# Kernel tuning notes

Hardware: AMD Instinct MI355X
Metric: run time of the kernel (lower is better)

## Reference

```python
import jax, jax.numpy as jnp
import numpy as np

N_NODES = 100000
N_FEAT = 128
N_EDGES = 640000
BATCH_SIZE = 50000


def setup_inputs() -> dict:
    key = jax.random.key(0)
    k1, k2 = jax.random.split(key)
    x = jax.random.normal(k1, (N_NODES, N_FEAT), dtype=jnp.float32)
    edge_index = jax.random.randint(k2, (2, N_EDGES), 0, N_NODES, dtype=jnp.int32)
    return {"x": x, "edge_index": edge_index, "batch_size": BATCH_SIZE}


def reference(x, edge_index, batch_size):
    # Filter edges whose destination is inside the target batch, then
    # scatter-sum source node features into destination rows (SpMM with a
    # 0/1 adjacency), matching adj.t().matmul(x) in the original.
    src = edge_index[0]
    dst = edge_index[1]
    valid = dst < batch_size                                  # [E]
    # Route invalid edges to a dummy segment (batch_size) and zero their values.
    seg = jnp.where(valid, dst, batch_size)                   # [E]
    vals = x[src] * valid[:, None].astype(x.dtype)            # [E, F] gather
    x_neighbors_sum = jax.ops.segment_sum(
        vals, seg, num_segments=batch_size + 1)[:batch_size]  # [B, F]
    node_labels = jnp.concatenate(
        [x[:batch_size, :], x_neighbors_sum], axis=-1)        # [B, 2F]
    return node_labels
```

## Files before the change

kernel.cpp:

```cpp
#include <hip/hip_runtime.h>

#define NFEAT 128
#define CAP 32
#define OVF_CAP 4096


__global__ void zero_kernel(int* __restrict__ p, int n) {
    int t = blockIdx.x * blockDim.x + threadIdx.x;
    if (t < n) p[t] = 0;
}

__global__ void bin_kernel(const int* __restrict__ src, const int* __restrict__ dst,
                           int* __restrict__ cnt, int* __restrict__ ovf_cnt,
                           int* __restrict__ ovf, int* __restrict__ bucket,
                           int E, int B) {
    int e = blockIdx.x * blockDim.x + threadIdx.x;
    if (e >= E) return;
    int d = dst[e];
    if (d >= B) return;
    int s = src[e];
    int pos = atomicAdd(&cnt[d], 1);
    if (pos < CAP) {
        bucket[d * CAP + pos] = s;
    } else {
        int o = atomicAdd(ovf_cnt, 1);
        if (o < OVF_CAP) { ovf[2 * o] = s; ovf[2 * o + 1] = d; }
    }
}

__global__ void aggregate_kernel(const float2* __restrict__ x2,
                                 const int* __restrict__ cnt,
                                 const int* __restrict__ bucket,
                                 float2* __restrict__ out2, int B) {
    int w = (blockIdx.x * blockDim.x + threadIdx.x) >> 6;
    int lane = threadIdx.x & 63;
    if (w >= B) return;
    int k = cnt[w];
    if (k > CAP) k = CAP;
    int sid = (lane < k) ? bucket[w * CAP + lane] : 0;
    float2 xd = x2[(size_t)w * 64 + lane];
    float2 acc = make_float2(0.f, 0.f);
    int j = 0;
    for (; j + 4 <= k; j += 4) {
        int s0 = __shfl(sid, j,     64);
        int s1 = __shfl(sid, j + 1, 64);
        int s2 = __shfl(sid, j + 2, 64);
        int s3 = __shfl(sid, j + 3, 64);
        float2 v0 = x2[(size_t)s0 * 64 + lane];
        float2 v1 = x2[(size_t)s1 * 64 + lane];
        float2 v2 = x2[(size_t)s2 * 64 + lane];
        float2 v3 = x2[(size_t)s3 * 64 + lane];
        acc.x += (v0.x + v1.x) + (v2.x + v3.x);
        acc.y += (v0.y + v1.y) + (v2.y + v3.y);
    }
    for (; j < k; ++j) {
        int s = __shfl(sid, j, 64);
        float2 v = x2[(size_t)s * 64 + lane];
        acc.x += v.x; acc.y += v.y;
    }
    size_t o = (size_t)w * 128;
    out2[o + lane] = xd;
    out2[o + 64 + lane] = acc;
}

__global__ void ovf_apply_kernel(const float* __restrict__ x,
                                 const int* __restrict__ ovf_cnt,
                                 const int* __restrict__ ovf,
                                 float* __restrict__ out, int B) {
    int n = *ovf_cnt;
    if (n > OVF_CAP) n = OVF_CAP;
    int t = blockIdx.x * blockDim.x + threadIdx.x;
    int e = t >> 5;
    if (e >= n) return;
    int c = t & 31;
    int s = ovf[2 * e], d = ovf[2 * e + 1];
    const float4 v = ((const float4*)(x + (size_t)s * NFEAT))[c];
    float* o = out + (size_t)d * 256 + NFEAT + c * 4;
    unsafeAtomicAdd(o + 0, v.x);
    unsafeAtomicAdd(o + 1, v.y);
    unsafeAtomicAdd(o + 2, v.z);
    unsafeAtomicAdd(o + 3, v.w);
}

__global__ void hist_kernel(const int* __restrict__ dst, int* __restrict__ cnt,
                            int E, int B) {
    int e = blockIdx.x * blockDim.x + threadIdx.x;
    if (e >= E) return;
    int d = dst[e];
    if (d < B) atomicAdd(&cnt[d], 1);
}

__global__ void alloc_kernel(const int* __restrict__ cnt, int* __restrict__ off,
                             int* __restrict__ deg, int* __restrict__ cursor, int B) {
    int t = blockIdx.x * blockDim.x + threadIdx.x;
    int lane = threadIdx.x & 63;
    int c = (t < B) ? cnt[t] : 0;
    int v = c;
    #pragma unroll
    for (int d = 1; d < 64; d <<= 1) {
        int n = __shfl_up(v, d, 64);
        if (lane >= d) v += n;
    }
    int total = __shfl(v, 63, 64);
    int base = 0;
    if (lane == 63 && total > 0) base = atomicAdd(cursor, total);
    base = __shfl(base, 63, 64);
    if (t < B) { off[t] = base + v - c; deg[t] = c; }
}

__global__ void scatter_kernel(const int* __restrict__ src, const int* __restrict__ dst,
                               int* __restrict__ cnt, const int* __restrict__ off,
                               int* __restrict__ bucket, int E, int B) {
    int e = blockIdx.x * blockDim.x + threadIdx.x;
    if (e >= E) return;
    int d = dst[e];
    if (d >= B) return;
    int old = atomicSub(&cnt[d], 1);
    bucket[off[d] + old - 1] = src[e];
}

__global__ void aggregate_csr_kernel(const float2* __restrict__ x2,
                                     const int* __restrict__ off, const int* __restrict__ deg,
                                     const int* __restrict__ bucket,
                                     float2* __restrict__ out2, int B) {
    int w = (blockIdx.x * blockDim.x + threadIdx.x) >> 6;
    int lane = threadIdx.x & 63;
    if (w >= B) return;
    int base = off[w];
    int k = deg[w];
    float2 acc = make_float2(0.f, 0.f);
    for (int j = 0; j < k; ++j) {
        int s = bucket[base + j];
        float2 v = x2[(size_t)s * 64 + lane];
        acc.x += v.x; acc.y += v.y;
    }
    float2 xd = x2[(size_t)w * 64 + lane];
    size_t o = (size_t)w * 128;
    out2[o + lane] = xd;
    out2[o + 64 + lane] = acc;
}

extern "C" void kernel_launch(void* const* d_in, const int* in_sizes, int n_in,
                              void* d_out, int out_size, void* d_ws, size_t ws_size,
                              hipStream_t stream) {
    const float* x  = (const float*)d_in[0];
    const int*   ei = (const int*)d_in[1];
    const int E = in_sizes[1] / 2;
    const int B = out_size / (2 * NFEAT);
    float* out = (float*)d_out;
    const int* src = ei;
    const int* dst = ei + E;

    size_t need_bin = ((size_t)B * (CAP + 1) + 1 + 2 * OVF_CAP) * sizeof(int);
    size_t need_csr = ((size_t)3 * B + 1 + E) * sizeof(int);

    if (ws_size >= need_bin) {
        int* cnt     = (int*)d_ws;
        int* ovf_cnt = cnt + B;
        int* ovf     = ovf_cnt + 1;
        int* bucket  = ovf + 2 * OVF_CAP;

        int nz = B + 1;
        zero_kernel<<<(nz + 255) / 256, 256, 0, stream>>>(cnt, nz);
        bin_kernel<<<(E + 255) / 256, 256, 0, stream>>>(src, dst, cnt, ovf_cnt, ovf, bucket, E, B);
        aggregate_kernel<<<(B + 3) / 4, 256, 0, stream>>>(
            (const float2*)x, cnt, bucket, (float2*)out, B);
        ovf_apply_kernel<<<(OVF_CAP * 32 + 255) / 256, 256, 0, stream>>>(x, ovf_cnt, ovf, out, B);
    } else {
        int* cnt    = (int*)d_ws;
        int* off    = cnt + B;
        int* deg    = off + B;
        int* cursor = deg + B;
        int* bucket = cursor + 1;
        int nz = 3 * B + 1;
        zero_kernel<<<(nz + 255) / 256, 256, 0, stream>>>(cnt, nz);
        hist_kernel<<<(E + 255) / 256, 256, 0, stream>>>(dst, cnt, E, B);
        alloc_kernel<<<(B + 255) / 256, 256, 0, stream>>>(cnt, off, deg, cursor, B);
        scatter_kernel<<<(E + 255) / 256, 256, 0, stream>>>(src, dst, cnt, off, bucket, E, B);
        aggregate_csr_kernel<<<(B + 3) / 4, 256, 0, stream>>>(
            (const float2*)x, off, deg, bucket, (float2*)out, B);
    }
}
```

Baseline: 140.7 us.

## Vectorize binning loads and process two rows per wavefront with float4 gathers

The bin kernel now handles four edges per thread using int4 loads of src and dst. The aggregate kernel splits each 64-lane wavefront into two halves, each gathering one destination row with float4 loads, so every load instruction moves more bytes and each wave covers two rows. Outputs are written with nontemporal stores. The cost is divergence when the two rows in a wave have different degrees, since both halves loop to the larger count, and the bin kernel runs with fewer threads, each issuing several atomics.

```diff
diff --git a/kernel.cpp b/kernel.cpp
--- a/kernel.cpp
+++ b/kernel.cpp
@@ -3,6 +3,8 @@
 #define NFEAT 128
 #define CAP 32
 #define OVF_CAP 4096
+
+typedef float vfloat4 __attribute__((ext_vector_type(4)));
 
 
 __global__ void zero_kernel(int* __restrict__ p, int n) {
@@ -14,53 +16,92 @@
                            int* __restrict__ cnt, int* __restrict__ ovf_cnt,
                            int* __restrict__ ovf, int* __restrict__ bucket,
                            int E, int B) {
-    int e = blockIdx.x * blockDim.x + threadIdx.x;
-    if (e >= E) return;
-    int d = dst[e];
-    if (d >= B) return;
-    int s = src[e];
-    int pos = atomicAdd(&cnt[d], 1);
-    if (pos < CAP) {
-        bucket[d * CAP + pos] = s;
+    int t = blockIdx.x * blockDim.x + threadIdx.x;
+    int e0 = t << 2;
+    if (e0 >= E) return;
+    if (e0 + 4 <= E) {
+        const int4 d4 = *(const int4*)(dst + e0);
+        const int4 s4 = *(const int4*)(src + e0);
+        int dd[4] = {d4.x, d4.y, d4.z, d4.w};
+        int ss[4] = {s4.x, s4.y, s4.z, s4.w};
+        #pragma unroll
+        for (int i = 0; i < 4; ++i) {
+            int d = dd[i];
+            if (d >= B) continue;
+            int pos = atomicAdd(&cnt[d], 1);
+            if (pos < CAP) {
+                bucket[d * CAP + pos] = ss[i];
+            } else {
+                int o = atomicAdd(ovf_cnt, 1);
+                if (o < OVF_CAP) { ovf[2 * o] = ss[i]; ovf[2 * o + 1] = d; }
+            }
+        }
     } else {
-        int o = atomicAdd(ovf_cnt, 1);
-        if (o < OVF_CAP) { ovf[2 * o] = s; ovf[2 * o + 1] = d; }
-    }
-}
-
-__global__ void aggregate_kernel(const float2* __restrict__ x2,
+        for (int e = e0; e < E; ++e) {
+            int d = dst[e];
+            if (d >= B) continue;
+            int pos = atomicAdd(&cnt[d], 1);
+            if (pos < CAP) {
+                bucket[d * CAP + pos] = src[e];
+            } else {
+                int o = atomicAdd(ovf_cnt, 1);
+                if (o < OVF_CAP) { ovf[2 * o] = src[e]; ovf[2 * o + 1] = d; }
+            }
+        }
+    }
+}
+
+__global__ void aggregate_kernel(const float4* __restrict__ x4,
                                  const int* __restrict__ cnt,
                                  const int* __restrict__ bucket,
-                                 float2* __restrict__ out2, int B) {
-    int w = (blockIdx.x * blockDim.x + threadIdx.x) >> 6;
+                                 float4* __restrict__ out4, int B) {
+    int wv   = (blockIdx.x * blockDim.x + threadIdx.x) >> 6;
     int lane = threadIdx.x & 63;
-    if (w >= B) return;
-    int k = cnt[w];
-    if (k > CAP) k = CAP;
-    int sid = (lane < k) ? bucket[w * CAP + lane] : 0;
-    float2 xd = x2[(size_t)w * 64 + lane];
-    float2 acc = make_float2(0.f, 0.f);
+    int h    = lane >> 5;
+    int l    = lane & 31;
+    int w0   = wv * 2;
+    if (w0 >= B) return;
+    int row   = w0 + h;
+    bool rowok = row < B;
+
+    int k = 0;
+    if (rowok) { k = cnt[row]; if (k > CAP) k = CAP; }
+    int sid = (l < k) ? bucket[(size_t)w0 * CAP + lane] : 0;
+    float4 xd = rowok ? x4[(size_t)row * 32 + l] : make_float4(0.f, 0.f, 0.f, 0.f);
+
+    int ko   = __shfl(k, lane ^ 32, 64);
+    int kmax = k > ko ? k : ko;
+
+    float4 acc = make_float4(0.f, 0.f, 0.f, 0.f);
+    int hb = h << 5;
     int j = 0;
-    for (; j + 4 <= k; j += 4) {
-        int s0 = __shfl(sid, j,     64);
-        int s1 = __shfl(sid, j + 1, 64);
-        int s2 = __shfl(sid, j + 2, 64);
-        int s3 = __shfl(sid, j + 3, 64);
-        float2 v0 = x2[(size_t)s0 * 64 + lane];
-        float2 v1 = x2[(size_t)s1 * 64 + lane];
-        float2 v2 = x2[(size_t)s2 * 64 + lane];
-        float2 v3 = x2[(size_t)s3 * 64 + lane];
-        acc.x += (v0.x + v1.x) + (v2.x + v3.x);
-        acc.y += (v0.y + v1.y) + (v2.y + v3.y);
-    }
-    for (; j < k; ++j) {
-        int s = __shfl(sid, j, 64);
-        float2 v = x2[(size_t)s * 64 + lane];
-        acc.x += v.x; acc.y += v.y;
-    }
-    size_t o = (size_t)w * 128;
-    out2[o + lane] = xd;
-    out2[o + 64 + lane] = acc;
+    for (; j + 4 <= kmax; j += 4) {
+        int s0 = __shfl(sid, hb + j,     64);
+        int s1 = __shfl(sid, hb + j + 1, 64);
+        int s2 = __shfl(sid, hb + j + 2, 64);
+        int s3 = __shfl(sid, hb + j + 3, 64);
+        float4 v0 = x4[(size_t)s0 * 32 + l];
+        float4 v1 = x4[(size_t)s1 * 32 + l];
+        float4 v2 = x4[(size_t)s2 * 32 + l];
+        float4 v3 = x4[(size_t)s3 * 32 + l];
+        if (j + 1 <= k) { acc.x += v0.x; acc.y += v0.y; acc.z += v0.z; acc.w += v0.w; }
+        if (j + 2 <= k) { acc.x += v1.x; acc.y += v1.y; acc.z += v1.z; acc.w += v1.w; }
+        if (j + 3 <= k) { acc.x += v2.x; acc.y += v2.y; acc.z += v2.z; acc.w += v2.w; }
+        if (j + 4 <= k) { acc.x += v3.x; acc.y += v3.y; acc.z += v3.z; acc.w += v3.w; }
+    }
+    for (; j < kmax; ++j) {
+        int s = __shfl(sid, hb + j, 64);
+        float4 v = x4[(size_t)s * 32 + l];
+        if (j < k) { acc.x += v.x; acc.y += v.y; acc.z += v.z; acc.w += v.w; }
+    }
+
+    if (rowok) {
+        size_t o = (size_t)row * 64;
+        vfloat4 xdn  = {xd.x, xd.y, xd.z, xd.w};
+        vfloat4 accn = {acc.x, acc.y, acc.z, acc.w};
+        __builtin_nontemporal_store(xdn,  (vfloat4*)&out4[o + l]);
+        __builtin_nontemporal_store(accn, (vfloat4*)&out4[o + 32 + l]);
+    }
 }
 
 __global__ void ovf_apply_kernel(const float* __restrict__ x,
@@ -162,9 +203,12 @@
 
         int nz = B + 1;
         zero_kernel<<<(nz + 255) / 256, 256, 0, stream>>>(cnt, nz);
-        bin_kernel<<<(E + 255) / 256, 256, 0, stream>>>(src, dst, cnt, ovf_cnt, ovf, bucket, E, B);
-        aggregate_kernel<<<(B + 3) / 4, 256, 0, stream>>>(
-            (const float2*)x, cnt, bucket, (float2*)out, B);
+        int nbin_threads = (E + 3) / 4;
+        bin_kernel<<<(nbin_threads + 255) / 256, 256, 0, stream>>>(
+            src, dst, cnt, ovf_cnt, ovf, bucket, E, B);
+        int npairs = (B + 1) / 2;
+        aggregate_kernel<<<(npairs + 3) / 4, 256, 0, stream>>>(
+            (const float4*)x, cnt, bucket, (float4*)out, B);
         ovf_apply_kernel<<<(OVF_CAP * 32 + 255) / 256, 256, 0, stream>>>(x, ovf_cnt, ovf, out, B);
     } else {
         int* cnt    = (int*)d_ws;
```

Result: no change. 141.2 us (+0.4%).
